# Performance work log

Hardware: AMD Instinct MI355X
Metric: run time of the kernel (lower is better)

The kernel has to match this reference:

```python
import jax, jax.numpy as jnp
import numpy as np

N, C, H, W_DIM = 32, 256, 64, 64


def setup_inputs() -> dict:
    key = jax.random.key(0)
    ks = jax.random.split(key, 7)
    x = jax.random.normal(ks[0], (N, C, H, W_DIM), dtype=jnp.float32)
    # 1x1 conv weights stored as 2-D matrices (out_ch, in_ch)
    W2 = jax.random.normal(ks[1], (C, C), dtype=jnp.float32) / np.sqrt(C).astype(np.float32)
    W8 = jax.random.normal(ks[2], (C, 25), dtype=jnp.float32) / np.sqrt(25.0).astype(np.float32)
    W10 = jax.random.normal(ks[3], (H * 25, C), dtype=jnp.float32) / np.sqrt(C).astype(np.float32)
    W18 = jax.random.normal(ks[4], (C * H,), dtype=jnp.float32)
    p4 = 0.02 * jax.random.normal(ks[5], (1, 1, H, W_DIM), dtype=jnp.float32)
    p13 = 0.02 * jax.random.normal(ks[6], (1, H, W_DIM), dtype=jnp.float32)
    return {"x": x, "W2": W2, "W8": W8, "W10": W10, "W18": W18, "p4": p4, "p13": p13}


def reference(x, W2, W8, W10, W18, p4, p13):
    n = x.shape[0]
    t1 = jax.nn.relu(x)                                  # (n,c,h,w)
    t2 = jnp.einsum('oc,nchw->nohw', W2, t1)             # 1x1 conv p_2
    t3 = t1.max(axis=(2, 3))                             # global max -> (n,c)
    t5 = (p4 * t2).mean(axis=1)                          # (n,h,w)
    # F.unfold(kernel=(5,5), dilation=3, padding=6): size-preserving dilated patches
    pad5 = jnp.pad(t5, ((0, 0), (6, 6), (6, 6)))
    t6 = jnp.stack(
        [pad5[:, 3 * ki:3 * ki + H, 3 * kj:3 * kj + W_DIM]
         for ki in range(5) for kj in range(5)],
        axis=1)                                          # (n,25,h,w), (ki,kj) row-major like torch
    t7 = t6.max(axis=2)                                  # max over h -> (n,25,w)
    t8 = jnp.einsum('ok,nkw->now', W8, t7)               # 1x1 conv p_8 -> (n,c,w)
    t9 = jnp.einsum('nc,nchw->nhw', t3, x)               # bmm global context -> (n,h,w)
    t10 = jnp.einsum('oc,ncw->now', W10, t8)             # 1x1 conv p_10 -> (n,25h,w)
    t11 = jax.nn.gelu(t10, approximate=False)            # torch F.gelu default = exact erf
    t12 = t6.reshape(n, 25 * H, W_DIM) + t11             # (n,25h,w)
    t13 = p13 * t9                                       # (n,h,w)
    t14 = jnp.exp(t12)
    # F.unfold(kernel=(1,7), dilation=(1,3), padding=(0,9)) along w, size-preserving
    padw = jnp.pad(t14, ((0, 0), (0, 0), (9, 9)))
    t15 = jnp.stack([padw[:, :, 3 * j:3 * j + W_DIM] for j in range(7)], axis=2)  # (n,25h,7,w)
    t16 = t15.max(axis=1)                                # (n,7,w)
    t17 = t16.mean(axis=1)                               # (n,w)
    t18 = W18[None, :, None] * t17[:, None, :]           # 1x1 conv p_18 (in_ch=1) -> (n,c*h,w)
    t19 = t13[:, None, :, :] - t18.reshape(n, C, H, W_DIM)
    return t19
```

## Files before the change

### kernel.cpp

```cpp
#include <hip/hip_runtime.h>
#include <math.h>

#define NB 32
#define C 256
#define H 64
#define W 64
#define HW 4096
#define K4_TILES 25

__global__ __launch_bounds__(256) void k1_t3_prep(
    const float* __restrict__ x, const float* __restrict__ W2,
    float* __restrict__ w2bar, float* __restrict__ t3) {
  int b = blockIdx.x;
  int tid = threadIdx.x;
  if (b == NB * C) {
    float s = 0.f;
    for (int o = 0; o < C; ++o) s += W2[o * C + tid];
    w2bar[tid] = s * (1.0f / (float)C);
    return;
  }
  const float4* xv = (const float4*)(x + (size_t)b * HW);
  float m = -3.4e38f;
#pragma unroll
  for (int i = 0; i < 4; ++i) {
    float4 v = xv[i * 256 + tid];
    m = fmaxf(m, fmaxf(fmaxf(v.x, v.y), fmaxf(v.z, v.w)));
  }
  for (int off = 32; off > 0; off >>= 1)
    m = fmaxf(m, __shfl_down(m, off, 64));
  __shared__ float sm[4];
  if ((tid & 63) == 0) sm[tid >> 6] = m;
  __syncthreads();
  if (tid == 0) {
    float mm = fmaxf(fmaxf(sm[0], sm[1]), fmaxf(sm[2], sm[3]));
    t3[b] = fmaxf(mm, 0.0f);
  }
}

__global__ __launch_bounds__(256) void k2_s_t9(
    const float* __restrict__ x, const float* __restrict__ w2bar,
    const float* __restrict__ t3, const float* __restrict__ p4,
    const float* __restrict__ p13, float* __restrict__ t5,
    float* __restrict__ t13) {
  int n = blockIdx.x >> 4;
  int p = ((blockIdx.x & 15) << 8) | threadIdx.x;
  __shared__ float sw[C];
  __shared__ float st[C];
  sw[threadIdx.x] = w2bar[threadIdx.x];
  st[threadIdx.x] = t3[n * C + threadIdx.x];
  __syncthreads();
  const float* xp = x + (size_t)n * C * HW + p;
  float accs = 0.f, acc9 = 0.f;
#pragma unroll 16
  for (int c = 0; c < C; ++c) {
    float v = xp[(size_t)c * HW];
    accs = fmaf(sw[c], fmaxf(v, 0.f), accs);
    acc9 = fmaf(st[c], v, acc9);
  }
  t5[n * HW + p] = p4[p] * accs;
  t13[n * HW + p] = p13[p] * acc9;
}

__global__ __launch_bounds__(256) void k3_t8(
    const float* __restrict__ t5, const float* __restrict__ W8,
    float* __restrict__ t8) {
  int n = blockIdx.x >> 2;
  int og = (blockIdx.x & 3) << 6;
  int tid = threadIdx.x;
  __shared__ float s5[HW];
  __shared__ float cm[5][64];
  __shared__ float t7s[25][64];
  const float4* t5v = (const float4*)(t5 + n * HW);
  float4* s5v = (float4*)s5;
#pragma unroll
  for (int i = 0; i < 4; ++i) s5v[i * 256 + tid] = t5v[i * 256 + tid];
  __syncthreads();
  for (int idx = tid; idx < 5 * 64; idx += 256) {
    int ki = idx >> 6, wp = idx & 63;
    int lo = max(0, 3 * ki - 6), hi = min(63, 3 * ki + 57);
    float m = (ki == 2) ? -3.4e38f : 0.0f;
    for (int hp = lo; hp <= hi; ++hp) m = fmaxf(m, s5[hp * 64 + wp]);
    cm[ki][wp] = m;
  }
  __syncthreads();
  for (int idx = tid; idx < 25 * 64; idx += 256) {
    int k = idx >> 6, w = idx & 63;
    int ki = k / 5, kj = k % 5;
    int wp = w + 3 * kj - 6;
    t7s[k][w] = (wp >= 0 && wp < 64) ? cm[ki][wp] : 0.0f;
  }
  __syncthreads();
  int w = tid & 63, orow = tid >> 6;
  for (int i = 0; i < 16; ++i) {
    int o = og + orow * 16 + i;
    float acc = 0.f;
#pragma unroll
    for (int k = 0; k < 25; ++k) acc = fmaf(W8[o * 25 + k], t7s[k][w], acc);
    t8[(n * C + o) * 64 + w] = acc;
  }
}

__global__ __launch_bounds__(256) void k4_t10max(
    const float* __restrict__ t8, const float* __restrict__ W10,
    const float* __restrict__ t5, float* __restrict__ part) {
  int n = blockIdx.x / K4_TILES;
  int tile = blockIdx.x - n * K4_TILES;
  int tid = threadIdx.x;
  int wg = tid & 15, w0 = wg * 4;
  int rg = tid >> 4;
  int o0 = tile * 64 + rg * 4;
  __shared__ float t8s[64 * 64];
  float4 acc[4];
#pragma unroll
  for (int j = 0; j < 4; ++j) acc[j] = make_float4(0.f, 0.f, 0.f, 0.f);
  const float4* w10v = (const float4*)W10;

  for (int ch = 0; ch < 4; ++ch) {
    const float4* src = (const float4*)(t8 + ((size_t)n * C + ch * 64) * 64);
    float4* dst = (float4*)t8s;
#pragma unroll
    for (int i = 0; i < 4; ++i) dst[i * 256 + tid] = src[i * 256 + tid];
    __syncthreads();
#pragma unroll 4
    for (int c4 = 0; c4 < 16; ++c4) {
      float4 tv0 = *(const float4*)&t8s[(c4 * 4 + 0) * 64 + w0];
      float4 tv1 = *(const float4*)&t8s[(c4 * 4 + 1) * 64 + w0];
      float4 tv2 = *(const float4*)&t8s[(c4 * 4 + 2) * 64 + w0];
      float4 tv3 = *(const float4*)&t8s[(c4 * 4 + 3) * 64 + w0];
#pragma unroll
      for (int j = 0; j < 4; ++j) {
        float4 a = w10v[(size_t)(o0 + j) * 64 + ch * 16 + c4];
        acc[j].x = fmaf(a.x, tv0.x, fmaf(a.y, tv1.x, fmaf(a.z, tv2.x, fmaf(a.w, tv3.x, acc[j].x))));
        acc[j].y = fmaf(a.x, tv0.y, fmaf(a.y, tv1.y, fmaf(a.z, tv2.y, fmaf(a.w, tv3.y, acc[j].y))));
        acc[j].z = fmaf(a.x, tv0.z, fmaf(a.y, tv1.z, fmaf(a.z, tv2.z, fmaf(a.w, tv3.z, acc[j].z))));
        acc[j].w = fmaf(a.x, tv0.w, fmaf(a.y, tv1.w, fmaf(a.z, tv2.w, fmaf(a.w, tv3.w, acc[j].w))));
      }
    }
    __syncthreads();
  }

  const float* t5n = t5 + n * HW;
  float pm[4] = {-3.4e38f, -3.4e38f, -3.4e38f, -3.4e38f};
#pragma unroll
  for (int j = 0; j < 4; ++j) {
    int o = o0 + j;
    int k = o >> 6, h = o & 63;
    int ki = k / 5, kj = k - ki * 5;
    int hp = h + 3 * ki - 6;
    float av[4] = {acc[j].x, acc[j].y, acc[j].z, acc[j].w};
#pragma unroll
    for (int e = 0; e < 4; ++e) {
      int wp = w0 + e + 3 * kj - 6;
      float t6v = (hp >= 0 && hp < 64 && wp >= 0 && wp < 64)
                      ? t5n[hp * 64 + wp] : 0.0f;
      float xg = av[e];
      float gl = 0.5f * xg * (1.0f + erff(xg * 0.70710678118654752f));
      pm[e] = fmaxf(pm[e], t6v + gl);
    }
  }
  float* red = t8s;
#pragma unroll
  for (int e = 0; e < 4; ++e) red[rg * 64 + w0 + e] = pm[e];
  __syncthreads();
  if (tid < 64) {
    float m = -3.4e38f;
#pragma unroll
    for (int g = 0; g < 16; ++g) m = fmaxf(m, red[g * 64 + tid]);
    part[(n * K4_TILES + tile) * 64 + tid] = m;
  }
}

__global__ __launch_bounds__(64) void k5_t17(
    const float* __restrict__ part, float* __restrict__ t17) {
  int n = blockIdx.x;
  int w = threadIdx.x;
  float m = -3.4e38f;
#pragma unroll
  for (int t = 0; t < K4_TILES; ++t)
    m = fmaxf(m, part[(n * K4_TILES + t) * 64 + w]);
  __shared__ float M[64];
  M[w] = expf(m);
  __syncthreads();
  float s = 0.f;
#pragma unroll
  for (int j = 0; j < 7; ++j) {
    int wp = w + 3 * j - 9;
    if (wp >= 0 && wp < 64) s += M[wp];
  }
  t17[n * 64 + w] = s * (1.0f / 7.0f);
}

__global__ __launch_bounds__(256) void k6_out(
    const float* __restrict__ t13, const float* __restrict__ t17,
    const float* __restrict__ W18, float* __restrict__ out) {
  int b = blockIdx.x;
  int n = b >> 8, c = b & 255;
  int tid = threadIdx.x;
  const float4* t13v = (const float4*)(t13 + n * HW);
  const float4* t17v = (const float4*)(t17 + n * 64);
  float4* outv = (float4*)(out + (size_t)b * HW);
#pragma unroll
  for (int i = 0; i < 4; ++i) {
    int idx = i * 256 + tid;
    int h = idx >> 4;
    int w4 = idx & 15;
    float w18 = W18[c * 64 + h];
    float4 a = t13v[idx];
    float4 tt = t17v[w4];
    float4 o;
    o.x = a.x - w18 * tt.x;
    o.y = a.y - w18 * tt.y;
    o.z = a.z - w18 * tt.z;
    o.w = a.w - w18 * tt.w;
    outv[idx] = o;
  }
}

extern "C" void kernel_launch(void* const* d_in, const int* in_sizes, int n_in,
                              void* d_out, int out_size, void* d_ws,
                              size_t ws_size, hipStream_t stream) {
  const float* x   = (const float*)d_in[0];
  const float* W2  = (const float*)d_in[1];
  const float* W8  = (const float*)d_in[2];
  const float* W10 = (const float*)d_in[3];
  const float* W18 = (const float*)d_in[4];
  const float* p4  = (const float*)d_in[5];
  const float* p13 = (const float*)d_in[6];
  float* out = (float*)d_out;

  float* ws    = (float*)d_ws;
  float* w2bar = ws;
  float* t3    = w2bar + 256;
  float* t5    = t3 + NB * C;
  float* t13   = t5 + NB * HW;
  float* t8    = t13 + NB * HW;
  float* part  = t8 + NB * C * 64;
  float* t17   = part + NB * K4_TILES * 64;

  k1_t3_prep<<<dim3(NB * C + 1), dim3(256), 0, stream>>>(x, W2, w2bar, t3);
  k2_s_t9<<<dim3(NB * 16), dim3(256), 0, stream>>>(x, w2bar, t3, p4, p13, t5, t13);
  k3_t8<<<dim3(NB * 4), dim3(256), 0, stream>>>(t5, W8, t8);
  k4_t10max<<<dim3(NB * K4_TILES), dim3(256), 0, stream>>>(t8, W10, t5, part);
  k5_t17<<<dim3(NB), dim3(64), 0, stream>>>(part, t17);
  k6_out<<<dim3(NB * C), dim3(256), 0, stream>>>(t13, t17, W18, out);
}
```

Measured before the change: 331.3 us.

## Precompose W10·W8 into one weight and fuse t8/t10 stages into one kernel

The change multiplies W10 by W8 once into a 1600x25 matrix, so t10 comes straight from the 25-row t7 and the intermediate t8 (n,256,64) is never built. The separate t8 kernel is merged into the t10/max kernel, which now takes the t6 values from shared-memory t5. This removes a 256-deep contraction per output and the t8 global round trip. In exchange a small weight-precompute kernel runs on every call, and summing in a different order changes floating-point rounding slightly.

```diff
diff --git a/kernel.cpp b/kernel.cpp
--- a/kernel.cpp
+++ b/kernel.cpp
@@ -6,7 +6,24 @@
 #define H 64
 #define W 64
 #define HW 4096
-#define K4_TILES 25
+#define KT 25
+
+__global__ __launch_bounds__(256) void k0_ww(
+    const float* __restrict__ W10, const float* __restrict__ W8,
+    float* __restrict__ WW) {
+  __shared__ float s8[256 * 25];
+  int tid = threadIdx.x;
+  for (int i = tid; i < 6400; i += 256) s8[i] = W8[i];
+  __syncthreads();
+  int idx = blockIdx.x * 256 + tid;
+  if (idx >= 1600 * 25) return;
+  int o = idx / 25, kk = idx - o * 25;
+  const float* wrow = W10 + (size_t)o * 256;
+  float acc = 0.f;
+#pragma unroll 8
+  for (int c = 0; c < 256; ++c) acc = fmaf(wrow[c], s8[c * 25 + kk], acc);
+  WW[idx] = acc;
+}
 
 __global__ __launch_bounds__(256) void k1_t3_prep(
     const float* __restrict__ x, const float* __restrict__ W2,
@@ -61,104 +78,78 @@
   t13[n * HW + p] = p13[p] * acc9;
 }
 
-__global__ __launch_bounds__(256) void k3_t8(
-    const float* __restrict__ t5, const float* __restrict__ W8,
-    float* __restrict__ t8) {
-  int n = blockIdx.x >> 2;
-  int og = (blockIdx.x & 3) << 6;
-  int tid = threadIdx.x;
+__global__ __launch_bounds__(256) void k4_fused(
+    const float* __restrict__ t5g, const float* __restrict__ WW,
+    float* __restrict__ part) {
+  int n = blockIdx.x / KT;
+  int k = blockIdx.x - n * KT;
+  int ki = k / 5, kj = k - ki * 5;
+  int tid = threadIdx.x;
+  int wg = tid & 15, w0 = wg * 4;
+  int rg = tid >> 4, h0 = rg * 4;
   __shared__ float s5[HW];
-  __shared__ float cm[5][64];
-  __shared__ float t7s[25][64];
-  const float4* t5v = (const float4*)(t5 + n * HW);
+  __shared__ float ww[64 * 25];
+  __shared__ float t7s[25 * 64];
+  __shared__ float cm[5 * 64];
+
+  const float4* t5v = (const float4*)(t5g + n * HW);
   float4* s5v = (float4*)s5;
 #pragma unroll
   for (int i = 0; i < 4; ++i) s5v[i * 256 + tid] = t5v[i * 256 + tid];
-  __syncthreads();
+  const float* wwsrc = WW + (size_t)k * 64 * 25;
+  for (int i = tid; i < 1600; i += 256) ww[i] = wwsrc[i];
+  __syncthreads();
+
   for (int idx = tid; idx < 5 * 64; idx += 256) {
-    int ki = idx >> 6, wp = idx & 63;
-    int lo = max(0, 3 * ki - 6), hi = min(63, 3 * ki + 57);
-    float m = (ki == 2) ? -3.4e38f : 0.0f;
+    int kii = idx >> 6, wp = idx & 63;
+    int lo = max(0, 3 * kii - 6), hi = min(63, 3 * kii + 57);
+    float m = (kii == 2) ? -3.4e38f : 0.0f;
     for (int hp = lo; hp <= hi; ++hp) m = fmaxf(m, s5[hp * 64 + wp]);
-    cm[ki][wp] = m;
+    cm[kii * 64 + wp] = m;
   }
   __syncthreads();
   for (int idx = tid; idx < 25 * 64; idx += 256) {
-    int k = idx >> 6, w = idx & 63;
-    int ki = k / 5, kj = k % 5;
-    int wp = w + 3 * kj - 6;
-    t7s[k][w] = (wp >= 0 && wp < 64) ? cm[ki][wp] : 0.0f;
-  }
-  __syncthreads();
-  int w = tid & 63, orow = tid >> 6;
-  for (int i = 0; i < 16; ++i) {
-    int o = og + orow * 16 + i;
-    float acc = 0.f;
-#pragma unroll
-    for (int k = 0; k < 25; ++k) acc = fmaf(W8[o * 25 + k], t7s[k][w], acc);
-    t8[(n * C + o) * 64 + w] = acc;
-  }
-}
-
-__global__ __launch_bounds__(256) void k4_t10max(
-    const float* __restrict__ t8, const float* __restrict__ W10,
-    const float* __restrict__ t5, float* __restrict__ part) {
-  int n = blockIdx.x / K4_TILES;
-  int tile = blockIdx.x - n * K4_TILES;
-  int tid = threadIdx.x;
-  int wg = tid & 15, w0 = wg * 4;
-  int rg = tid >> 4;
-  int o0 = tile * 64 + rg * 4;
-  __shared__ float t8s[64 * 64];
+    int kk = idx >> 6, w = idx & 63;
+    int kki = kk / 5, kkj = kk - kki * 5;
+    int wp = w + 3 * kkj - 6;
+    t7s[kk * 64 + w] = (wp >= 0 && wp < 64) ? cm[kki * 64 + wp] : 0.0f;
+  }
+  __syncthreads();
+
   float4 acc[4];
 #pragma unroll
   for (int j = 0; j < 4; ++j) acc[j] = make_float4(0.f, 0.f, 0.f, 0.f);
-  const float4* w10v = (const float4*)W10;
-
-  for (int ch = 0; ch < 4; ++ch) {
-    const float4* src = (const float4*)(t8 + ((size_t)n * C + ch * 64) * 64);
-    float4* dst = (float4*)t8s;
-#pragma unroll
-    for (int i = 0; i < 4; ++i) dst[i * 256 + tid] = src[i * 256 + tid];
-    __syncthreads();
-#pragma unroll 4
-    for (int c4 = 0; c4 < 16; ++c4) {
-      float4 tv0 = *(const float4*)&t8s[(c4 * 4 + 0) * 64 + w0];
-      float4 tv1 = *(const float4*)&t8s[(c4 * 4 + 1) * 64 + w0];
-      float4 tv2 = *(const float4*)&t8s[(c4 * 4 + 2) * 64 + w0];
-      float4 tv3 = *(const float4*)&t8s[(c4 * 4 + 3) * 64 + w0];
-#pragma unroll
-      for (int j = 0; j < 4; ++j) {
-        float4 a = w10v[(size_t)(o0 + j) * 64 + ch * 16 + c4];
-        acc[j].x = fmaf(a.x, tv0.x, fmaf(a.y, tv1.x, fmaf(a.z, tv2.x, fmaf(a.w, tv3.x, acc[j].x))));
-        acc[j].y = fmaf(a.x, tv0.y, fmaf(a.y, tv1.y, fmaf(a.z, tv2.y, fmaf(a.w, tv3.y, acc[j].y))));
-        acc[j].z = fmaf(a.x, tv0.z, fmaf(a.y, tv1.z, fmaf(a.z, tv2.z, fmaf(a.w, tv3.z, acc[j].z))));
-        acc[j].w = fmaf(a.x, tv0.w, fmaf(a.y, tv1.w, fmaf(a.z, tv2.w, fmaf(a.w, tv3.w, acc[j].w))));
-      }
+#pragma unroll
+  for (int kk = 0; kk < 25; ++kk) {
+    float4 tv = *(const float4*)&t7s[kk * 64 + w0];
+#pragma unroll
+    for (int j = 0; j < 4; ++j) {
+      float a = ww[(h0 + j) * 25 + kk];
+      acc[j].x = fmaf(a, tv.x, acc[j].x);
+      acc[j].y = fmaf(a, tv.y, acc[j].y);
+      acc[j].z = fmaf(a, tv.z, acc[j].z);
+      acc[j].w = fmaf(a, tv.w, acc[j].w);
     }
-    __syncthreads();
-  }
-
-  const float* t5n = t5 + n * HW;
+  }
+
+  int hpb = 3 * ki - 6, wpb = 3 * kj - 6;
   float pm[4] = {-3.4e38f, -3.4e38f, -3.4e38f, -3.4e38f};
 #pragma unroll
   for (int j = 0; j < 4; ++j) {
-    int o = o0 + j;
-    int k = o >> 6, h = o & 63;
-    int ki = k / 5, kj = k - ki * 5;
-    int hp = h + 3 * ki - 6;
+    int hp = h0 + j + hpb;
     float av[4] = {acc[j].x, acc[j].y, acc[j].z, acc[j].w};
 #pragma unroll
     for (int e = 0; e < 4; ++e) {
-      int wp = w0 + e + 3 * kj - 6;
+      int wp = w0 + e + wpb;
       float t6v = (hp >= 0 && hp < 64 && wp >= 0 && wp < 64)
-                      ? t5n[hp * 64 + wp] : 0.0f;
+                      ? s5[hp * 64 + wp] : 0.0f;
       float xg = av[e];
       float gl = 0.5f * xg * (1.0f + erff(xg * 0.70710678118654752f));
       pm[e] = fmaxf(pm[e], t6v + gl);
     }
   }
-  float* red = t8s;
+  __syncthreads();
+  float* red = t7s;
 #pragma unroll
   for (int e = 0; e < 4; ++e) red[rg * 64 + w0 + e] = pm[e];
   __syncthreads();
@@ -166,7 +157,7 @@
     float m = -3.4e38f;
 #pragma unroll
     for (int g = 0; g < 16; ++g) m = fmaxf(m, red[g * 64 + tid]);
-    part[(n * K4_TILES + tile) * 64 + tid] = m;
+    part[(n * KT + k) * 64 + tid] = m;
   }
 }
 
@@ -176,8 +167,8 @@
   int w = threadIdx.x;
   float m = -3.4e38f;
 #pragma unroll
-  for (int t = 0; t < K4_TILES; ++t)
-    m = fmaxf(m, part[(n * K4_TILES + t) * 64 + w]);
+  for (int t = 0; t < KT; ++t)
+    m = fmaxf(m, part[(n * KT + t) * 64 + w]);
   __shared__ float M[64];
   M[w] = expf(m);
   __syncthreads();
@@ -233,14 +224,14 @@
   float* t3    = w2bar + 256;
   float* t5    = t3 + NB * C;
   float* t13   = t5 + NB * HW;
-  float* t8    = t13 + NB * HW;
-  float* part  = t8 + NB * C * 64;
-  float* t17   = part + NB * K4_TILES * 64;
-
+  float* WW    = t13 + NB * HW;
+  float* part  = WW + 1600 * 25;
+  float* t17   = part + NB * KT * 64;
+
+  k0_ww<<<dim3(157), dim3(256), 0, stream>>>(W10, W8, WW);
   k1_t3_prep<<<dim3(NB * C + 1), dim3(256), 0, stream>>>(x, W2, w2bar, t3);
   k2_s_t9<<<dim3(NB * 16), dim3(256), 0, stream>>>(x, w2bar, t3, p4, p13, t5, t13);
-  k3_t8<<<dim3(NB * 4), dim3(256), 0, stream>>>(t5, W8, t8);
-  k4_t10max<<<dim3(NB * K4_TILES), dim3(256), 0, stream>>>(t8, W10, t5, part);
+  k4_fused<<<dim3(NB * KT), dim3(256), 0, stream>>>(t5, WW, part);
   k5_t17<<<dim3(NB), dim3(64), 0, stream>>>(part, t17);
   k6_out<<<dim3(NB * C), dim3(256), 0, stream>>>(t13, t17, W18, out);
 }
```

Measured after the change: 311.5 us. -6.0%, faster.
